# Optimization experiments

Measured on AMD Instinct MI355X. Metric: run time of the kernel, lower is better.

Reference implementation:

```python
import jax, jax.numpy as jnp
import numpy as np

S = 128          # shared sequence length of v/q/a/k
D = 512          # model dim
H = 8            # n_heads
W = D // H       # head width (becomes the v/q/a einsum axes)
NUM = S // 8     # num_v = num_q = num_a = num_k
SCALE = float(np.sqrt(H))  # source divides by sqrt(a.size(-1)) == sqrt(n_heads)


def _heads(x):
    # split_last(x,(H,-1)).transpose(1,2) on a 2D (S,D) tensor -> (S, W, H)
    return x.reshape(S, H, W).transpose(0, 2, 1)


def setup_inputs() -> dict:
    key = jax.random.key(0)
    ks = jax.random.split(key, 24)
    d = {}
    for i, n in enumerate(['v', 'q', 'a', 'k']):
        d[n] = jax.random.normal(ks[i], (S, D), jnp.float32)
    for n in ['v_mask', 'q_mask', 'a_mask', 'k_mask']:
        d[n] = jnp.ones((S,), jnp.bool_)
    wnames = ['Wv', 'Wq', 'Wa', 'Wk', 'Wvo', 'Wqo', 'Wao', 'Wko']
    bnames = ['bv', 'bq', 'ba', 'bk', 'bvo', 'bqo', 'bao', 'bko']
    for i, (wn, bn) in enumerate(zip(wnames, bnames)):
        d[wn] = jax.random.normal(ks[4 + 2 * i], (D, D), jnp.float32) / np.sqrt(D)
        d[bn] = jax.random.normal(ks[5 + 2 * i], (D,), jnp.float32) * 0.01
    return d


def reference(v, q, a, k, v_mask, q_mask, a_mask, k_mask,
              Wv, bv, Wq, bq, Wa, ba, Wk, bk,
              Wvo, bvo, Wqo, bqo, Wao, bao, Wko, bko):
    # input projections (torch Linear: x @ W.T + b)
    vp = v @ Wv.T + bv
    qp = q @ Wq.T + bq
    ap = a @ Wa.T + ba
    kp = k @ Wk.T + bk
    # output projections are applied to the already-projected tensors
    vo = vp @ Wvo.T + bvo
    qo = qp @ Wqo.T + bqo
    ao = ap @ Wao.T + bao
    ko = kp @ Wko.T + bko
    tv, tq, ta, tk = map(_heads, (vp, qp, ap, kp))      # (S, W, H)
    tvo, tqo, tao, tko = map(_heads, (vo, qo, ao, ko))  # (S, W, H)
    # trilinear scores: in source labels b=1, h=S, v/q/a in W, w=H
    att = jnp.einsum('sic,sjc,slc->sijl', tv, tq, ta) / SCALE   # (S, W, W, W)
    att1 = jnp.einsum('sic,sjc,slc->sijl', tv, tq, tk) / SCALE  # (S, W, W, W)
    # joint softmax over the flat num_v*num_q*num_a axis (flat memory reshape,
    # exactly like torch .view); dropout p=0.0 -> identity
    scores = jax.nn.softmax(att.reshape(-1, H, NUM * NUM * NUM), axis=-1)
    scores = scores.reshape(-1, H, NUM, NUM, NUM)  # stored as self.scores in torch
    # output contractions use the UNNORMALIZED att1 (as in the source)
    v_res = jnp.einsum('sijl,sic->isc', att1, tvo).reshape(1, W, S * H)
    q_res = jnp.einsum('sijl,sjc->jsc', att1, tqo).reshape(1, W, S * H)
    a_res = jnp.einsum('sijl,slc->lsc', att1, tao).reshape(1, W, S * H)
    k_res = tko[None].reshape(1, S, W * H)
    return (v_res, q_res, a_res, k_res, scores)
```

## Files before the change

kernel.cpp:

```cpp
#include <hip/hip_runtime.h>
#include <hip/hip_bf16.h>

#define INV_SCALE 0.35355339059327373f

struct Proj4Args {
  const float* x[4];
  const float* w[4];
  const float* b[4];
  float* y[4];
};

__device__ __forceinline__ void proj_body(const Proj4Args& A, int blk, int t,
                                          float* SH) {
  const int p = blk >> 6;
  const int dbase = (blk & 63) * 8;
  const int s = t & 127;
  const int h = t >> 7;
  float* WL = SH;
  float(*XT)[129] = (float(*)[129])(SH + 4096);
  {
    const float4* wg = (const float4*)(A.w[p] + dbase * 512);
    float4* wl4 = (float4*)WL;
#pragma unroll
    for (int r = 0; r < 4; ++r) wl4[t + r * 256] = wg[t + r * 256];
  }
  const float* xg = A.x[p];
  const int row = t >> 3;
  const int col = t & 7;
  float acc[4] = {0.f, 0.f, 0.f, 0.f};
  float4 pre[4];
#pragma unroll
  for (int r = 0; r < 4; ++r)
    pre[r] = ((const float4*)(xg + (row + r * 32) * 512))[col];
  for (int c = 0; c < 16; ++c) {
    __syncthreads();
#pragma unroll
    for (int r = 0; r < 4; ++r) {
      float4 f = pre[r];
      int rr = row + r * 32;
      XT[col * 4 + 0][rr] = f.x;
      XT[col * 4 + 1][rr] = f.y;
      XT[col * 4 + 2][rr] = f.z;
      XT[col * 4 + 3][rr] = f.w;
    }
    __syncthreads();
    if (c + 1 < 16) {
#pragma unroll
      for (int r = 0; r < 4; ++r)
        pre[r] = ((const float4*)(xg + (row + r * 32) * 512))[(c + 1) * 8 + col];
    }
#pragma unroll
    for (int k4 = 0; k4 < 8; ++k4) {
      float xv0 = XT[k4 * 4 + 0][s];
      float xv1 = XT[k4 * 4 + 1][s];
      float xv2 = XT[k4 * 4 + 2][s];
      float xv3 = XT[k4 * 4 + 3][s];
#pragma unroll
      for (int di = 0; di < 4; ++di) {
        const float4 wv =
            *(const float4*)&WL[(h * 4 + di) * 512 + c * 32 + k4 * 4];
        acc[di] = fmaf(wv.x, xv0, acc[di]);
        acc[di] = fmaf(wv.y, xv1, acc[di]);
        acc[di] = fmaf(wv.z, xv2, acc[di]);
        acc[di] = fmaf(wv.w, xv3, acc[di]);
      }
    }
  }
  const float* bp = A.b[p];
  float4 o;
  o.x = acc[0] + bp[dbase + h * 4 + 0];
  o.y = acc[1] + bp[dbase + h * 4 + 1];
  o.z = acc[2] + bp[dbase + h * 4 + 2];
  o.w = acc[3] + bp[dbase + h * 4 + 3];
  *(float4*)(A.y[p] + s * 512 + dbase + h * 4) = o;
}

__global__ __launch_bounds__(256) void proj4_kernel(Proj4Args A) {
  __shared__ float SH[8224];
  proj_body(A, blockIdx.x, threadIdx.x, SH);
}

__device__ __forceinline__ void scores_body(const float* __restrict__ vp,
                                            const float* __restrict__ qp,
                                            const float* __restrict__ ap,
                                            float* __restrict__ out, int b,
                                            int t, float* SH) {
  const int s = b >> 4;
  const int i0 = (b & 15) * 4;
  float* tqL = SH;
  float* taL = SH + 512;
  float* uL = SH + 1024;
  float(*redM)[4] = (float(*)[4])(SH + 1056);
  float(*redS)[4] = (float(*)[4])(SH + 1072);
  {
    const float* qr = qp + s * 512;
    const float* ar = ap + s * 512;
    tqL[t] = qr[t]; tqL[t + 256] = qr[t + 256];
    taL[t] = ar[t]; taL[t + 256] = ar[t + 256];
    if (t < 32) {
      int ii = t >> 3, c = t & 7;
      uL[t] = vp[s * 512 + c * 64 + i0 + ii] * INV_SCALE;
    }
  }
  __syncthreads();
  const int j0 = t >> 3;
  const int l0 = (t & 7) * 8;
  float acc[4][16];
#pragma unroll
  for (int ii = 0; ii < 4; ++ii)
#pragma unroll
    for (int x = 0; x < 16; ++x) acc[ii][x] = 0.f;
#pragma unroll
  for (int c = 0; c < 8; ++c) {
    float t0 = tqL[c * 64 + j0];
    float t1 = tqL[c * 64 + j0 + 32];
    float4 A0 = *reinterpret_cast<const float4*>(&taL[c * 64 + l0]);
    float4 A1v = *reinterpret_cast<const float4*>(&taL[c * 64 + l0 + 4]);
    float ta8[8] = {A0.x, A0.y, A0.z, A0.w, A1v.x, A1v.y, A1v.z, A1v.w};
#pragma unroll
    for (int ii = 0; ii < 4; ++ii) {
      float uv = uL[ii * 8 + c];
      float m0 = uv * t0;
      float m1 = uv * t1;
#pragma unroll
      for (int x = 0; x < 8; ++x) {
        acc[ii][x] = fmaf(m0, ta8[x], acc[ii][x]);
        acc[ii][8 + x] = fmaf(m1, ta8[x], acc[ii][8 + x]);
      }
    }
  }
  const int wid = t >> 6, ln = t & 63;
#pragma unroll
  for (int ii = 0; ii < 4; ++ii) {
    float m = acc[ii][0];
#pragma unroll
    for (int x = 1; x < 16; ++x) m = fmaxf(m, acc[ii][x]);
#pragma unroll
    for (int o = 32; o; o >>= 1) m = fmaxf(m, __shfl_xor(m, o));
    if (ln == 0) redM[ii][wid] = m;
  }
  __syncthreads();
#pragma unroll
  for (int ii = 0; ii < 4; ++ii) {
    float mf = fmaxf(fmaxf(redM[ii][0], redM[ii][1]),
                     fmaxf(redM[ii][2], redM[ii][3]));
    float sl = 0.f;
#pragma unroll
    for (int x = 0; x < 16; ++x) {
      float e = __expf(acc[ii][x] - mf);
      acc[ii][x] = e;
      sl += e;
    }
#pragma unroll
    for (int o = 32; o; o >>= 1) sl += __shfl_xor(sl, o);
    if (ln == 0) redS[ii][wid] = sl;
  }
  __syncthreads();
  const long sbase = 262144L + (long)s * 262144 + (long)i0 * 4096;
#pragma unroll
  for (int ii = 0; ii < 4; ++ii) {
    float tot = (redS[ii][0] + redS[ii][1]) + (redS[ii][2] + redS[ii][3]);
    float sc = 1.0f / tot;
#pragma unroll
    for (int jj = 0; jj < 2; ++jj) {
      float4* pp = reinterpret_cast<float4*>(
          out + sbase + ii * 4096 + (j0 + jj * 32) * 64 + l0);
      pp[0] = make_float4(acc[ii][jj * 8 + 0] * sc, acc[ii][jj * 8 + 1] * sc,
                          acc[ii][jj * 8 + 2] * sc, acc[ii][jj * 8 + 3] * sc);
      pp[1] = make_float4(acc[ii][jj * 8 + 4] * sc, acc[ii][jj * 8 + 5] * sc,
                          acc[ii][jj * 8 + 6] * sc, acc[ii][jj * 8 + 7] * sc);
    }
  }
}

struct FusedArgs {
  Proj4Args pj;
  const float* vp;
  const float* qp;
  const float* ap;
  float* out;
};

__global__ __launch_bounds__(256) void fused_kernel(FusedArgs F) {
  __shared__ float SH[8224];
  const int b = blockIdx.x;
  if (b < 2048)
    scores_body(F.vp, F.qp, F.ap, F.out, b, threadIdx.x, SH);
  else
    proj_body(F.pj, b - 2048, threadIdx.x, SH);
}

__global__ __launch_bounds__(256) void post_kernel(
    const float* __restrict__ vp, const float* __restrict__ qp,
    const float* __restrict__ kp, const float* __restrict__ vo,
    const float* __restrict__ qo, const float* __restrict__ ao,
    const float* __restrict__ ko, float* __restrict__ out) {
  const int s = blockIdx.x;
  const int t = threadIdx.x;
  const int wid = t >> 6;
  const int ln = t & 63;
  __shared__ float Ssum[3][8];
  const float* srcs[3] = {vp, qp, kp};
#pragma unroll
  for (int tt = 0; tt < 3; ++tt) {
    const float* r = srcs[tt] + s * 512;
    float a = r[wid * 64 + ln];
    float b = r[256 + wid * 64 + ln];
#pragma unroll
    for (int o = 32; o; o >>= 1) {
      a += __shfl_xor(a, o);
      b += __shfl_xor(b, o);
    }
    if (ln == 0) { Ssum[tt][wid] = a; Ssum[tt][wid + 4] = b; }
  }
  __syncthreads();
  if (wid == 3) {
    float tmp[8];
#pragma unroll
    for (int h = 0; h < 8; ++h)
      tmp[h] = ko[s * 512 + h * 64 + ln];
    float4* pp = reinterpret_cast<float4*>(out + 196608 + (s * 64 + ln) * 8);
    pp[0] = make_float4(tmp[0], tmp[1], tmp[2], tmp[3]);
    pp[1] = make_float4(tmp[4], tmp[5], tmp[6], tmp[7]);
  } else {
    const float* base = (wid == 0) ? vp : (wid == 1) ? qp : kp;
    const float* obase = (wid == 0) ? vo : (wid == 1) ? qo : ao;
    const int c0 = (wid == 0) ? 1 : 0;
    const int c1 = (wid == 2) ? 1 : 2;
    float A1 = 0.f;
#pragma unroll
    for (int c = 0; c < 8; ++c)
      A1 += base[s * 512 + c * 64 + ln] * (Ssum[c0][c] * Ssum[c1][c]);
    A1 *= INV_SCALE;
    float tmp[8];
#pragma unroll
    for (int c = 0; c < 8; ++c)
      tmp[c] = obase[s * 512 + c * 64 + ln] * A1;
    float4* pp = reinterpret_cast<float4*>(out + wid * 65536 + (ln * 128 + s) * 8);
    pp[0] = make_float4(tmp[0], tmp[1], tmp[2], tmp[3]);
    pp[1] = make_float4(tmp[4], tmp[5], tmp[6], tmp[7]);
  }
}

extern "C" void kernel_launch(void* const* d_in, const int* in_sizes, int n_in,
                              void* d_out, int out_size, void* d_ws, size_t ws_size,
                              hipStream_t stream) {
  int wb = 8;
  if (n_in >= 5 && in_sizes[4] == 262144) wb = 4;
  const float* W[8];
  const float* B[8];
  for (int i = 0; i < 8; ++i) {
    W[i] = (const float*)d_in[wb + 2 * i];
    B[i] = (const float*)d_in[wb + 2 * i + 1];
  }
  float* ws = (float*)d_ws;
  float* vp = ws;
  float* qp = ws + 65536;
  float* ap = ws + 131072;
  float* kp = ws + 196608;
  float* vo = ws + 262144;
  float* qo = ws + 327680;
  float* ao = ws + 393216;
  float* ko = ws + 458752;
  float* out = (float*)d_out;

  Proj4Args a1;
  for (int i = 0; i < 4; ++i) {
    a1.x[i] = (const float*)d_in[i];
    a1.w[i] = W[i];
    a1.b[i] = B[i];
  }
  a1.y[0] = vp; a1.y[1] = qp; a1.y[2] = ap; a1.y[3] = kp;
  hipLaunchKernelGGL(proj4_kernel, dim3(256), dim3(256), 0, stream, a1);

  FusedArgs F;
  F.pj.x[0] = vp; F.pj.x[1] = qp; F.pj.x[2] = ap; F.pj.x[3] = kp;
  for (int i = 0; i < 4; ++i) {
    F.pj.w[i] = W[4 + i];
    F.pj.b[i] = B[4 + i];
  }
  F.pj.y[0] = vo; F.pj.y[1] = qo; F.pj.y[2] = ao; F.pj.y[3] = ko;
  F.vp = vp; F.qp = qp; F.ap = ap; F.out = out;
  hipLaunchKernelGGL(fused_kernel, dim3(2304), dim3(256), 0, stream, F);

  hipLaunchKernelGGL(post_kernel, dim3(128), dim3(256), 0, stream,
                     vp, qp, kp, vo, qo, ao, ko, out);
}
```

Baseline: 240.1 us.

## Fuse output projections with result contraction, drop post kernel

The second projection GEMM now computes the per-head sums and the att1 contraction factor itself, and writes v/q/a/k results directly to the output in the final layout. This removes the separate post kernel launch and the workspace round trip for vo/qo/ao/ko. Projection blocks are moved to the front of the fused grid so they schedule ahead of the scores blocks. In exchange, each projection block redundantly recomputes the row head sums and performs scattered strided stores.

After: 233.0 us. 2.9% less time.

```diff
diff --git a/kernel.cpp b/kernel.cpp
--- a/kernel.cpp
+++ b/kernel.cpp
@@ -10,21 +10,19 @@
   float* y[4];
 };
 
-__device__ __forceinline__ void proj_body(const Proj4Args& A, int blk, int t,
-                                          float* SH) {
-  const int p = blk >> 6;
-  const int dbase = (blk & 63) * 8;
+__device__ __forceinline__ void gemm8_body(const float* xg, const float* wg_p,
+                                           const float* bp, int dbase, int t,
+                                           float* SH, float o[4]) {
   const int s = t & 127;
   const int h = t >> 7;
   float* WL = SH;
   float(*XT)[129] = (float(*)[129])(SH + 4096);
   {
-    const float4* wg = (const float4*)(A.w[p] + dbase * 512);
+    const float4* wg = (const float4*)(wg_p + dbase * 512);
     float4* wl4 = (float4*)WL;
 #pragma unroll
     for (int r = 0; r < 4; ++r) wl4[t + r * 256] = wg[t + r * 256];
   }
-  const float* xg = A.x[p];
   const int row = t >> 3;
   const int col = t & 7;
   float acc[4] = {0.f, 0.f, 0.f, 0.f};
@@ -66,18 +64,85 @@
       }
     }
   }
-  const float* bp = A.b[p];
-  float4 o;
-  o.x = acc[0] + bp[dbase + h * 4 + 0];
-  o.y = acc[1] + bp[dbase + h * 4 + 1];
-  o.z = acc[2] + bp[dbase + h * 4 + 2];
-  o.w = acc[3] + bp[dbase + h * 4 + 3];
-  *(float4*)(A.y[p] + s * 512 + dbase + h * 4) = o;
+#pragma unroll
+  for (int di = 0; di < 4; ++di) o[di] = acc[di] + bp[dbase + h * 4 + di];
 }
 
 __global__ __launch_bounds__(256) void proj4_kernel(Proj4Args A) {
   __shared__ float SH[8224];
-  proj_body(A, blockIdx.x, threadIdx.x, SH);
+  const int blk = blockIdx.x;
+  const int p = blk >> 6;
+  const int dbase = (blk & 63) * 8;
+  const int t = threadIdx.x;
+  float o[4];
+  gemm8_body(A.x[p], A.w[p], A.b[p], dbase, t, SH, o);
+  const int s = t & 127;
+  const int h = t >> 7;
+  *(float4*)(A.y[p] + s * 512 + dbase + h * 4) = make_float4(o[0], o[1], o[2], o[3]);
+}
+
+struct FusedArgs {
+  const float* w2[4];
+  const float* b2[4];
+  const float* vp;
+  const float* qp;
+  const float* ap;
+  const float* kp;
+  float* out;
+};
+
+__device__ __forceinline__ void proj2_direct_body(const FusedArgs& F, int blk,
+                                                  int t, float* SH) {
+  const int p = blk >> 6;
+  const int dbase = (blk & 63) * 8;
+  const float* xsrc[4] = {F.vp, F.qp, F.ap, F.kp};
+  float o[4];
+  gemm8_body(xsrc[p], F.w2[p], F.b2[p], dbase, t, SH, o);
+  const int s = t & 127;
+  const int h = t >> 7;
+  const int c_head = dbase >> 6;
+  const int i0 = (dbase & 63) + h * 4;
+  if (p == 3) {
+#pragma unroll
+    for (int di = 0; di < 4; ++di)
+      F.out[196608 + s * 512 + (i0 + di) * 8 + c_head] = o[di];
+    return;
+  }
+  const float* fac = (p == 0) ? F.vp : (p == 1) ? F.qp : F.kp;
+  const float* S0 = (p == 0) ? F.qp : F.vp;
+  const float* S1 = (p == 2) ? F.qp : F.kp;
+  __syncthreads();
+  float* Sm = SH;
+#pragma unroll
+  for (int m = 0; m < 2; ++m) {
+    const float* M = m ? S1 : S0;
+#pragma unroll
+    for (int cc = 0; cc < 4; ++cc) {
+      const int c = h * 4 + cc;
+      const float4* r4 = (const float4*)(M + s * 512 + c * 64);
+      float sum = 0.f;
+#pragma unroll
+      for (int u = 0; u < 16; ++u) {
+        float4 f = r4[u];
+        sum += (f.x + f.y) + (f.z + f.w);
+      }
+      Sm[m * 1024 + s * 8 + c] = sum;
+    }
+  }
+  __syncthreads();
+  float prod[8];
+#pragma unroll
+  for (int c = 0; c < 8; ++c)
+    prod[c] = Sm[s * 8 + c] * Sm[1024 + s * 8 + c];
+#pragma unroll
+  for (int di = 0; di < 4; ++di) {
+    const int i = i0 + di;
+    float A1 = 0.f;
+#pragma unroll
+    for (int c = 0; c < 8; ++c)
+      A1 = fmaf(fac[s * 512 + c * 64 + i], prod[c], A1);
+    F.out[p * 65536 + i * 1024 + s * 8 + c_head] = o[di] * (A1 * INV_SCALE);
+  }
 }
 
 __device__ __forceinline__ void scores_body(const float* __restrict__ vp,
@@ -173,73 +238,13 @@
   }
 }
 
-struct FusedArgs {
-  Proj4Args pj;
-  const float* vp;
-  const float* qp;
-  const float* ap;
-  float* out;
-};
-
 __global__ __launch_bounds__(256) void fused_kernel(FusedArgs F) {
   __shared__ float SH[8224];
   const int b = blockIdx.x;
-  if (b < 2048)
-    scores_body(F.vp, F.qp, F.ap, F.out, b, threadIdx.x, SH);
+  if (b < 256)
+    proj2_direct_body(F, b, threadIdx.x, SH);
   else
-    proj_body(F.pj, b - 2048, threadIdx.x, SH);
-}
-
-__global__ __launch_bounds__(256) void post_kernel(
-    const float* __restrict__ vp, const float* __restrict__ qp,
-    const float* __restrict__ kp, const float* __restrict__ vo,
-    const float* __restrict__ qo, const float* __restrict__ ao,
-    const float* __restrict__ ko, float* __restrict__ out) {
-  const int s = blockIdx.x;
-  const int t = threadIdx.x;
-  const int wid = t >> 6;
-  const int ln = t & 63;
-  __shared__ float Ssum[3][8];
-  const float* srcs[3] = {vp, qp, kp};
-#pragma unroll
-  for (int tt = 0; tt < 3; ++tt) {
-    const float* r = srcs[tt] + s * 512;
-    float a = r[wid * 64 + ln];
-    float b = r[256 + wid * 64 + ln];
-#pragma unroll
-    for (int o = 32; o; o >>= 1) {
-      a += __shfl_xor(a, o);
-      b += __shfl_xor(b, o);
-    }
-    if (ln == 0) { Ssum[tt][wid] = a; Ssum[tt][wid + 4] = b; }
-  }
-  __syncthreads();
-  if (wid == 3) {
-    float tmp[8];
-#pragma unroll
-    for (int h = 0; h < 8; ++h)
-      tmp[h] = ko[s * 512 + h * 64 + ln];
-    float4* pp = reinterpret_cast<float4*>(out + 196608 + (s * 64 + ln) * 8);
-    pp[0] = make_float4(tmp[0], tmp[1], tmp[2], tmp[3]);
-    pp[1] = make_float4(tmp[4], tmp[5], tmp[6], tmp[7]);
-  } else {
-    const float* base = (wid == 0) ? vp : (wid == 1) ? qp : kp;
-    const float* obase = (wid == 0) ? vo : (wid == 1) ? qo : ao;
-    const int c0 = (wid == 0) ? 1 : 0;
-    const int c1 = (wid == 2) ? 1 : 2;
-    float A1 = 0.f;
-#pragma unroll
-    for (int c = 0; c < 8; ++c)
-      A1 += base[s * 512 + c * 64 + ln] * (Ssum[c0][c] * Ssum[c1][c]);
-    A1 *= INV_SCALE;
-    float tmp[8];
-#pragma unroll
-    for (int c = 0; c < 8; ++c)
-      tmp[c] = obase[s * 512 + c * 64 + ln] * A1;
-    float4* pp = reinterpret_cast<float4*>(out + wid * 65536 + (ln * 128 + s) * 8);
-    pp[0] = make_float4(tmp[0], tmp[1], tmp[2], tmp[3]);
-    pp[1] = make_float4(tmp[4], tmp[5], tmp[6], tmp[7]);
-  }
+    scores_body(F.vp, F.qp, F.ap, F.out, b - 256, threadIdx.x, SH);
 }
 
 extern "C" void kernel_launch(void* const* d_in, const int* in_sizes, int n_in,
@@ -258,10 +263,6 @@
   float* qp = ws + 65536;
   float* ap = ws + 131072;
   float* kp = ws + 196608;
-  float* vo = ws + 262144;
-  float* qo = ws + 327680;
-  float* ao = ws + 393216;
-  float* ko = ws + 458752;
   float* out = (float*)d_out;
 
   Proj4Args a1;
@@ -274,15 +275,10 @@
   hipLaunchKernelGGL(proj4_kernel, dim3(256), dim3(256), 0, stream, a1);
 
   FusedArgs F;
-  F.pj.x[0] = vp; F.pj.x[1] = qp; F.pj.x[2] = ap; F.pj.x[3] = kp;
   for (int i = 0; i < 4; ++i) {
-    F.pj.w[i] = W[4 + i];
-    F.pj.b[i] = B[4 + i];
-  }
-  F.pj.y[0] = vo; F.pj.y[1] = qo; F.pj.y[2] = ao; F.pj.y[3] = ko;
-  F.vp = vp; F.qp = qp; F.ap = ap; F.out = out;
+    F.w2[i] = W[4 + i];
+    F.b2[i] = B[4 + i];
+  }
+  F.vp = vp; F.qp = qp; F.ap = ap; F.kp = kp; F.out = out;
   hipLaunchKernelGGL(fused_kernel, dim3(2304), dim3(256), 0, stream, F);
-
-  hipLaunchKernelGGL(post_kernel, dim3(128), dim3(256), 0, stream,
-                     vp, qp, kp, vo, qo, ao, ko, out);
-}
+}
```
